# Performance work log

Hardware: AMD Instinct MI355X
Metric: run time of the kernel (lower is better)

Reference implementation:

```python
import jax, jax.numpy as jnp
import numpy as np

B, T, H, NSPK = 8, 1024, 1024, 2
LN_EPS = 1e-5


def setup_inputs() -> dict:
    key = jax.random.key(0)
    ks = jax.random.split(key, 12)
    s = 1.0 / np.sqrt(H)
    return {
        "x": jax.random.normal(ks[0], (B, T, H), jnp.float32),
        "qmask": jax.random.uniform(ks[1], (B, T, NSPK), jnp.float32),
        "dia_len": jax.random.randint(ks[2], (B,), T // 2, T + 1),
        "wp": 8,
        "wf": 8,
        "W_msg": jax.random.normal(ks[3], (H, H), jnp.float32) * s,
        "b_msg": jax.random.normal(ks[4], (H,), jnp.float32) * s,
        "W_self": jax.random.normal(ks[5], (H, H), jnp.float32) * s,
        "b_self": jax.random.normal(ks[6], (H,), jnp.float32) * s,
        "W_out": jax.random.normal(ks[7], (H, H), jnp.float32) * s,
        "b_out": jax.random.normal(ks[8], (H,), jnp.float32) * s,
        "gamma": jnp.ones((H,), jnp.float32),
        "beta": jnp.zeros((H,), jnp.float32),
    }


def reference(x, qmask, dia_len, wp, wf, W_msg, b_msg, W_self, b_self, W_out, b_out, gamma, beta):
    Bb, Tt, Hh = x.shape
    spk = jnp.argmax(qmask, axis=-1)                     # [B,T]
    pos = jnp.arange(Tt)
    offs = jnp.arange(-wp, wf + 1)                       # [W]
    idx = pos[:, None] + offs[None, :]                   # [T,W] window indices
    vlen = dia_len[:, None, None]                        # [B,1,1]
    valid = (idx[None] >= 0) & (idx[None] <= vlen - 1)   # [B,T,W]
    idxc = jnp.clip(idx, 0, Tt - 1)
    nb = jnp.take(x, idxc, axis=1)                       # [B,T,W,H]
    nb_spk = jnp.take(spk, idxc, axis=1)                 # [B,T,W]
    same = (nb_spk == spk[:, :, None]).astype(x.dtype)
    w = jnp.where(valid, 0.5 + 0.5 * same, 0.0)          # speaker weights, masked
    cnt = jnp.maximum(valid.sum(-1).astype(x.dtype), 1.0)  # window sizes [B,T]
    msg = jnp.einsum('btw,btwh->bth', w, nb) / cnt[..., None]
    h = x @ W_self + b_self + msg @ W_msg + b_msg        # per-node fusion
    node_valid = (pos[None, :] < dia_len[:, None])[..., None]
    out = jnp.where(node_valid, h, x)                    # nodes past dia_len keep x
    y = jax.nn.relu(out) @ W_out + b_out                 # dropout = identity (eval)
    z = x + y
    mean = z.mean(-1, keepdims=True)
    var = z.var(-1, keepdims=True)
    return gamma * (z - mean) / jnp.sqrt(var + LN_EPS) + beta
```

## Files before the change

kernel.cpp:

```cpp
#include <hip/hip_runtime.h>


typedef unsigned short u16;
typedef float floatx4 __attribute__((ext_vector_type(4)));
typedef short shortx8 __attribute__((ext_vector_type(8)));

#define T_ 1024
#define H_ 1024

__device__ __forceinline__ float bf2f(u16 v) {
    return __uint_as_float(((unsigned)v) << 16);
}
__device__ __forceinline__ u16 f2bf(float f) {
    unsigned u = __float_as_uint(f);
    return (u16)((u + 0x7fffu + ((u >> 16) & 1u)) >> 16);
}
__device__ __forceinline__ void async16(const void* g, void* l) {
    __builtin_amdgcn_global_load_lds(
        (__attribute__((address_space(1))) void*)g,
        (__attribute__((address_space(3))) void*)l, 16, 0, 0);
}
__device__ __forceinline__ void barrier_mem() {
    asm volatile("" ::: "memory");
    __builtin_amdgcn_s_barrier();
    asm volatile("" ::: "memory");
}

__global__ __launch_bounds__(256)
void prep_kernel(const float* __restrict__ x, const float* __restrict__ qmask,
                 const int* __restrict__ dia_len,
                 const float* __restrict__ Wself, const float* __restrict__ Wmsg,
                 const float* __restrict__ Wout,
                 u16* __restrict__ xcat, u16* __restrict__ wt_cat,
                 u16* __restrict__ wt_out)
{
    __shared__ u16 sx[32][1024];
    const int tid = threadIdx.x;
    const int bx = blockIdx.x;

    if (bx >= 512) {
        const int id = bx - 512;
        const int wid = id >> 10;
        const int rest = id & 1023;
        const int n0 = (rest & 31) * 32, k0 = (rest >> 5) * 32;
        const float* src = (wid == 0) ? Wself : ((wid == 1) ? Wmsg : Wout);
        float (*s)[33] = reinterpret_cast<float (*)[33]>(&sx[0][0]);
        const int tx = tid & 31, ty = tid >> 5;
#pragma unroll
        for (int i = 0; i < 4; ++i) {
            int k = k0 + ty + 8 * i;
            s[ty + 8 * i][tx] = src[(size_t)k * H_ + n0 + tx];
        }
        __syncthreads();
#pragma unroll
        for (int i = 0; i < 4; ++i) {
            int n = n0 + ty + 8 * i;
            u16 v = f2bf(s[tx][ty + 8 * i]);
            if (wid < 2) wt_cat[(size_t)n * 2048 + wid * 1024 + k0 + tx] = v;
            else         wt_out[(size_t)n * 1024 + k0 + tx] = v;
        }
        return;
    }

    const int b = bx >> 6;
    const int t0 = (bx & 63) * 16;
    const int dlen = dia_len[b];
    const int c4 = tid * 4;
    const float* xb = x + (size_t)b * T_ * H_;

    unsigned spkmask = 0;
#pragma unroll 4
    for (int r = 0; r < 32; ++r) {
        int row = t0 - 8 + r;
        row = row < 0 ? 0 : (row > T_ - 1 ? T_ - 1 : row);
        const float* q = qmask + ((size_t)b * T_ + row) * 2;
        spkmask |= (q[1] > q[0] ? 1u : 0u) << r;
        float4 v = *(const float4*)(xb + (size_t)row * H_ + c4);
        ushort4 u;
        u.x = f2bf(v.x); u.y = f2bf(v.y); u.z = f2bf(v.z); u.w = f2bf(v.w);
        *(ushort4*)&sx[r][c4] = u;
    }
    __syncthreads();

    for (int lt = 0; lt < 16; ++lt) {
        const int t = t0 + lt;
        const unsigned cs = (spkmask >> (lt + 8)) & 1u;
        float a0 = 0.f, a1 = 0.f, a2 = 0.f, a3 = 0.f;
        int cnt = 0;
#pragma unroll
        for (int o = 0; o < 17; ++o) {
            const int idx = t + o - 8;
            if (idx >= 0 && idx < dlen) {
                const float w = (((spkmask >> (lt + o)) & 1u) == cs) ? 1.0f : 0.5f;
                ++cnt;
                ushort4 u = *(const ushort4*)&sx[lt + o][c4];
                a0 += w * bf2f(u.x); a1 += w * bf2f(u.y);
                a2 += w * bf2f(u.z); a3 += w * bf2f(u.w);
            }
        }
        const float inv = 1.0f / (float)(cnt > 0 ? cnt : 1);
        ushort4 m;
        m.x = f2bf(a0 * inv); m.y = f2bf(a1 * inv);
        m.z = f2bf(a2 * inv); m.w = f2bf(a3 * inv);
        const size_t rowg = (size_t)b * T_ + t;
        *(ushort4*)&xcat[rowg * 2048 + 1024 + c4] = m;
        *(ushort4*)&xcat[rowg * 2048 + c4] = *(const ushort4*)&sx[lt + 8][c4];
    }
}


#define LOADSET(AV, BV, TT) do {                                              \
    const u16* pA_ = &sA[(TT) & 3][0];                                        \
    const u16* pB_ = &sB[(TT) & 3][0];                                        \
    AV[0] = *(const shortx8*)(pA_ + aOff0);                                   \
    AV[1] = *(const shortx8*)(pA_ + aOff1);                                   \
    BV[0] = *(const shortx8*)(pB_ + bOff0);                                   \
    BV[1] = *(const shortx8*)(pB_ + bOff1);                                   \
    BV[2] = *(const shortx8*)(pB_ + bOff2);                                   \
    BV[3] = *(const shortx8*)(pB_ + bOff3);                                   \
} while (0)

#define GBODY(TT, AC, BC, AN, BNV) do {                                       \
    if ((TT) + 1 < NT) LOADSET(AN, BNV, (TT) + 1);                            \
    if ((TT) + 3 < NT) stage((TT) + 3);                                       \
    __builtin_amdgcn_sched_barrier(0);                                        \
    __builtin_amdgcn_s_setprio(1);                                            \
    acc[0][0] = __builtin_amdgcn_mfma_f32_16x16x32_bf16(AC[0], BC[0], acc[0][0], 0, 0, 0); \
    acc[1][0] = __builtin_amdgcn_mfma_f32_16x16x32_bf16(AC[1], BC[0], acc[1][0], 0, 0, 0); \
    acc[0][1] = __builtin_amdgcn_mfma_f32_16x16x32_bf16(AC[0], BC[1], acc[0][1], 0, 0, 0); \
    acc[1][1] = __builtin_amdgcn_mfma_f32_16x16x32_bf16(AC[1], BC[1], acc[1][1], 0, 0, 0); \
    acc[0][2] = __builtin_amdgcn_mfma_f32_16x16x32_bf16(AC[0], BC[2], acc[0][2], 0, 0, 0); \
    acc[1][2] = __builtin_amdgcn_mfma_f32_16x16x32_bf16(AC[1], BC[2], acc[1][2], 0, 0, 0); \
    acc[0][3] = __builtin_amdgcn_mfma_f32_16x16x32_bf16(AC[0], BC[3], acc[0][3], 0, 0, 0); \
    acc[1][3] = __builtin_amdgcn_mfma_f32_16x16x32_bf16(AC[1], BC[3], acc[1][3], 0, 0, 0); \
    __builtin_amdgcn_s_setprio(0);                                            \
    if ((TT) + 1 < NT) {                                                      \
        if ((TT) + 3 < NT) asm volatile("s_waitcnt vmcnt(2)" ::: "memory");   \
        else               asm volatile("s_waitcnt vmcnt(0)" ::: "memory");   \
        barrier_mem();                                                        \
    }                                                                         \
} while (0)

template <int K, int EPI>
__global__ __launch_bounds__(512, 4)
void gemm_bt(const u16* __restrict__ A, const u16* __restrict__ Bt,
             const float* __restrict__ bias1, const float* __restrict__ bias2,
             const float* __restrict__ X, const int* __restrict__ dia_len,
             u16* __restrict__ Rout, float* __restrict__ Zout)
{
    constexpr int NT = K / 32;
    static_assert(NT >= 4 && (NT & 1) == 0, "NT even, >=4");
    __shared__ u16 sA[4][128 * 32];
    __shared__ u16 sB[4][128 * 32];
    const int tid = threadIdx.x;

    const int bid = blockIdx.x;
    const int xcd = bid & 7, li = bid >> 3;
    const int mt = xcd * 8 + (li >> 3);
    const int nt = li & 7;
    const int bm = mt * 128, bn = nt * 128;

    const int wave = tid >> 6, lane = tid & 63;
    const int wr = wave >> 1, wc = wave & 1;
    const int lrow = lane & 15, lq = lane >> 4;

    const int srow = tid >> 2;
    const int sl   = (tid & 3) ^ ((srow >> 1) & 3);
    const u16* Asrc = A + (size_t)(bm + srow) * K + sl * 8;
    const u16* Bsrc = Bt + (size_t)(bn + srow) * K + sl * 8;

    auto stage = [&](int t) {
        const int s = t & 3;
        async16(Asrc + t * 32, &sA[s][tid * 8]);
        async16(Bsrc + t * 32, &sB[s][tid * 8]);
    };

    floatx4 acc[2][4];
#pragma unroll
    for (int i = 0; i < 2; ++i)
#pragma unroll
        for (int j = 0; j < 4; ++j)
            acc[i][j] = (floatx4){0.f, 0.f, 0.f, 0.f};

    const int ra0 = wr * 32 + lrow,      ra1 = ra0 + 16;
    const int rb0 = wc * 64 + lrow,      rb1 = rb0 + 16,
              rb2 = rb0 + 32,            rb3 = rb0 + 48;
    const int aOff0 = ra0 * 32 + (lq ^ ((ra0 >> 1) & 3)) * 8;
    const int aOff1 = ra1 * 32 + (lq ^ ((ra1 >> 1) & 3)) * 8;
    const int bOff0 = rb0 * 32 + (lq ^ ((rb0 >> 1) & 3)) * 8;
    const int bOff1 = rb1 * 32 + (lq ^ ((rb1 >> 1) & 3)) * 8;
    const int bOff2 = rb2 * 32 + (lq ^ ((rb2 >> 1) & 3)) * 8;
    const int bOff3 = rb3 * 32 + (lq ^ ((rb3 >> 1) & 3)) * 8;

    stage(0); stage(1); stage(2);
    asm volatile("s_waitcnt vmcnt(2)" ::: "memory");
    barrier_mem();

    shortx8 aP[2], bP[4], aQ[2], bQ[4];
    LOADSET(aP, bP, 0);

    for (int t = 0; t < NT; t += 2) {
        GBODY(t,     aP, bP, aQ, bQ);
        GBODY(t + 1, aQ, bQ, aP, bP);
    }

    const int dl = (EPI == 1) ? dia_len[bm >> 10] : 0;
#pragma unroll
    for (int i = 0; i < 2; ++i) {
        const int row0 = bm + wr * 32 + i * 16 + lq * 4;
#pragma unroll
        for (int j = 0; j < 4; ++j) {
            const int col = bn + wc * 64 + j * 16 + lrow;
#pragma unroll
            for (int r = 0; r < 4; ++r) {
                const int row = row0 + r;
                const float v = acc[i][j][r];
                if (EPI == 1) {
                    const float h = v + bias1[col] + bias2[col];
                    float outv;
                    if ((row & (T_ - 1)) < dl) {
                        outv = h;
                    } else {
                        outv = X[(size_t)row * H_ + col];
                    }
                    Rout[(size_t)row * H_ + col] = f2bf(fmaxf(outv, 0.f));
                } else {
                    const float z = X[(size_t)row * H_ + col] + v + bias1[col];
                    Zout[(size_t)row * H_ + col] = z;
                }
            }
        }
    }
}

__global__ __launch_bounds__(256)
void ln_kernel(const float* __restrict__ Z, const float* __restrict__ gamma,
               const float* __restrict__ beta, float* __restrict__ out)
{
    const int row = blockIdx.x;
    const int tid = threadIdx.x;
    const size_t base = (size_t)row * H_ + tid * 4;
    float4 v = *(const float4*)(Z + base);
    float s = v.x + v.y + v.z + v.w;
    float q = v.x * v.x + v.y * v.y + v.z * v.z + v.w * v.w;
#pragma unroll
    for (int off = 32; off > 0; off >>= 1) {
        s += __shfl_down(s, off);
        q += __shfl_down(q, off);
    }
    __shared__ float ps[4], pq[4];
    const int wave = tid >> 6, lane = tid & 63;
    if (lane == 0) { ps[wave] = s; pq[wave] = q; }
    __syncthreads();
    const float S = ps[0] + ps[1] + ps[2] + ps[3];
    const float Q = pq[0] + pq[1] + pq[2] + pq[3];
    const float mean = S * (1.0f / 1024.0f);
    const float var = Q * (1.0f / 1024.0f) - mean * mean;
    const float inv = rsqrtf(var + 1e-5f);
    float4 g = *(const float4*)(gamma + tid * 4);
    float4 bt = *(const float4*)(beta + tid * 4);
    float4 o;
    o.x = g.x * (v.x - mean) * inv + bt.x;
    o.y = g.y * (v.y - mean) * inv + bt.y;
    o.z = g.z * (v.z - mean) * inv + bt.z;
    o.w = g.w * (v.w - mean) * inv + bt.w;
    *(float4*)(out + base) = o;
}

extern "C" void kernel_launch(void* const* d_in, const int* in_sizes, int n_in,
                              void* d_out, int out_size, void* d_ws, size_t ws_size,
                              hipStream_t stream)
{
    (void)in_sizes; (void)n_in; (void)out_size; (void)ws_size;
    const float* x       = (const float*)d_in[0];
    const float* qmask   = (const float*)d_in[1];
    const int*   dia_len = (const int*)d_in[2];
    const float* W_msg   = (const float*)d_in[5];
    const float* b_msg   = (const float*)d_in[6];
    const float* W_self  = (const float*)d_in[7];
    const float* b_self  = (const float*)d_in[8];
    const float* W_out   = (const float*)d_in[9];
    const float* b_out   = (const float*)d_in[10];
    const float* gamma   = (const float*)d_in[11];
    const float* beta    = (const float*)d_in[12];
    float* out = (float*)d_out;

    char* ws = (char*)d_ws;
    u16*   xcat   = (u16*)ws;
    u16*   rbuf   = (u16*)(ws + (size_t)(32u << 20));
    u16*   wt_cat = (u16*)(ws + (size_t)(48u << 20));
    u16*   wt_out = (u16*)(ws + (size_t)(52u << 20));
    float* zbuf   = (float*)ws;

    prep_kernel<<<dim3(3584), 256, 0, stream>>>(x, qmask, dia_len,
                                                W_self, W_msg, W_out,
                                                xcat, wt_cat, wt_out);
    gemm_bt<2048, 1><<<dim3(512), 512, 0, stream>>>(xcat, wt_cat, b_self, b_msg,
                                                    x, dia_len, rbuf, nullptr);
    gemm_bt<1024, 2><<<dim3(512), 512, 0, stream>>>(rbuf, wt_out, b_out, nullptr,
                                                    x, nullptr, nullptr, zbuf);
    ln_kernel<<<dim3(8192), 256, 0, stream>>>(zbuf, gamma, beta, out);
}
```

Before: 210.7 us.

## Load GEMM B operand directly from global into registers, bypass LDS

B-tile fragments are now read from global memory straight into each wave's registers instead of being staged asynchronously into LDS. Only A stays in LDS, now triple-buffered. The stage prefetch moves after the barrier, and the wait count becomes vmcnt(1). This frees LDS and drops the B LDS reads, but each of the four row-waves now fetches the same B data separately from global/L2. The tighter wait also exposes more global load latency in the MFMA loop.

```diff
diff --git a/kernel.cpp b/kernel.cpp
--- a/kernel.cpp
+++ b/kernel.cpp
@@ -109,20 +109,24 @@
 }
 
 
-#define LOADSET(AV, BV, TT) do {                                              \
-    const u16* pA_ = &sA[(TT) & 3][0];                                        \
-    const u16* pB_ = &sB[(TT) & 3][0];                                        \
+#define LOADB(BV, TT) do {                                                    \
+    BV[0] = *(const shortx8*)(bBase0 + (size_t)(TT) * 32);                    \
+    BV[1] = *(const shortx8*)(bBase1 + (size_t)(TT) * 32);                    \
+    BV[2] = *(const shortx8*)(bBase2 + (size_t)(TT) * 32);                    \
+    BV[3] = *(const shortx8*)(bBase3 + (size_t)(TT) * 32);                    \
+} while (0)
+
+#define LOADA(AV, TT) do {                                                    \
+    const u16* pA_ = &sA[(TT) % 3][0];                                        \
     AV[0] = *(const shortx8*)(pA_ + aOff0);                                   \
     AV[1] = *(const shortx8*)(pA_ + aOff1);                                   \
-    BV[0] = *(const shortx8*)(pB_ + bOff0);                                   \
-    BV[1] = *(const shortx8*)(pB_ + bOff1);                                   \
-    BV[2] = *(const shortx8*)(pB_ + bOff2);                                   \
-    BV[3] = *(const shortx8*)(pB_ + bOff3);                                   \
 } while (0)
 
 #define GBODY(TT, AC, BC, AN, BNV) do {                                       \
-    if ((TT) + 1 < NT) LOADSET(AN, BNV, (TT) + 1);                            \
-    if ((TT) + 3 < NT) stage((TT) + 3);                                       \
+    if ((TT) + 1 < NT) {                                                      \
+        LOADB(BNV, (TT) + 1);                                                 \
+        LOADA(AN, (TT) + 1);                                                  \
+    }                                                                         \
     __builtin_amdgcn_sched_barrier(0);                                        \
     __builtin_amdgcn_s_setprio(1);                                            \
     acc[0][0] = __builtin_amdgcn_mfma_f32_16x16x32_bf16(AC[0], BC[0], acc[0][0], 0, 0, 0); \
@@ -135,9 +139,9 @@
     acc[1][3] = __builtin_amdgcn_mfma_f32_16x16x32_bf16(AC[1], BC[3], acc[1][3], 0, 0, 0); \
     __builtin_amdgcn_s_setprio(0);                                            \
     if ((TT) + 1 < NT) {                                                      \
-        if ((TT) + 3 < NT) asm volatile("s_waitcnt vmcnt(2)" ::: "memory");   \
-        else               asm volatile("s_waitcnt vmcnt(0)" ::: "memory");   \
+        asm volatile("s_waitcnt vmcnt(1)" ::: "memory");                      \
         barrier_mem();                                                        \
+        if ((TT) + 3 < NT) stage((TT) + 3);                                   \
     }                                                                         \
 } while (0)
 
@@ -150,8 +154,7 @@
 {
     constexpr int NT = K / 32;
     static_assert(NT >= 4 && (NT & 1) == 0, "NT even, >=4");
-    __shared__ u16 sA[4][128 * 32];
-    __shared__ u16 sB[4][128 * 32];
+    __shared__ u16 sA[3][128 * 32];
     const int tid = threadIdx.x;
 
     const int bid = blockIdx.x;
@@ -167,13 +170,15 @@
     const int srow = tid >> 2;
     const int sl   = (tid & 3) ^ ((srow >> 1) & 3);
     const u16* Asrc = A + (size_t)(bm + srow) * K + sl * 8;
-    const u16* Bsrc = Bt + (size_t)(bn + srow) * K + sl * 8;
 
     auto stage = [&](int t) {
-        const int s = t & 3;
-        async16(Asrc + t * 32, &sA[s][tid * 8]);
-        async16(Bsrc + t * 32, &sB[s][tid * 8]);
+        async16(Asrc + (size_t)t * 32, &sA[t % 3][tid * 8]);
     };
+
+    const u16* bBase0 = Bt + (size_t)(bn + wc * 64 +  0 + lrow) * K + lq * 8;
+    const u16* bBase1 = Bt + (size_t)(bn + wc * 64 + 16 + lrow) * K + lq * 8;
+    const u16* bBase2 = Bt + (size_t)(bn + wc * 64 + 32 + lrow) * K + lq * 8;
+    const u16* bBase3 = Bt + (size_t)(bn + wc * 64 + 48 + lrow) * K + lq * 8;
 
     floatx4 acc[2][4];
 #pragma unroll
@@ -182,22 +187,16 @@
         for (int j = 0; j < 4; ++j)
             acc[i][j] = (floatx4){0.f, 0.f, 0.f, 0.f};
 
-    const int ra0 = wr * 32 + lrow,      ra1 = ra0 + 16;
-    const int rb0 = wc * 64 + lrow,      rb1 = rb0 + 16,
-              rb2 = rb0 + 32,            rb3 = rb0 + 48;
+    const int ra0 = wr * 32 + lrow, ra1 = ra0 + 16;
     const int aOff0 = ra0 * 32 + (lq ^ ((ra0 >> 1) & 3)) * 8;
     const int aOff1 = ra1 * 32 + (lq ^ ((ra1 >> 1) & 3)) * 8;
-    const int bOff0 = rb0 * 32 + (lq ^ ((rb0 >> 1) & 3)) * 8;
-    const int bOff1 = rb1 * 32 + (lq ^ ((rb1 >> 1) & 3)) * 8;
-    const int bOff2 = rb2 * 32 + (lq ^ ((rb2 >> 1) & 3)) * 8;
-    const int bOff3 = rb3 * 32 + (lq ^ ((rb3 >> 1) & 3)) * 8;
 
     stage(0); stage(1); stage(2);
-    asm volatile("s_waitcnt vmcnt(2)" ::: "memory");
+    shortx8 aP[2], bP[4], aQ[2], bQ[4];
+    LOADB(bP, 0);
+    asm volatile("s_waitcnt vmcnt(0)" ::: "memory");
     barrier_mem();
-
-    shortx8 aP[2], bP[4], aQ[2], bQ[4];
-    LOADSET(aP, bP, 0);
+    LOADA(aP, 0);
 
     for (int t = 0; t < NT; t += 2) {
         GBODY(t,     aP, bP, aQ, bQ);
```

Result: slower. 343.2 us (+62.9%).
